# Kernel tuning notes

Hardware: AMD Instinct MI355X
Metric: run time of the kernel (lower is better)

The kernel has to match this reference:

```python
import jax, jax.numpy as jnp
import numpy as np

SIZE_IMG = 512
STRIDE = 32
N_ANCHOR = 9
BOUND_AC_LO, BOUND_AC_HI = -0.2, 1.2
EPS = 1e-05
IOU_SCALE = 10000
NEG_TH_ACGT = int(IOU_SCALE * 0.3)
POS_TH_ACGT = int(IOU_SCALE * 0.5)
POS_TH_GTAC = int(IOU_SCALE * 0.01)
NUM_POS_RPN = 128
NUM_NEG_RPN = 128
B, N_GT = 512, 32


def _anchors_rel(size_img, stride):
    h_fm = w_fm = size_img // stride
    # scales: closest floor power of 2 of min image side
    smax = 2 ** (size_img).bit_length()
    scales = np.array([smax >> 3, smax >> 2, smax >> 1], dtype=np.float32)
    sqrt2 = 1.4142135624
    ratio_hw = np.array([[sqrt2, sqrt2 / 2], [1, 1], [sqrt2 / 2, sqrt2]], dtype=np.float32)
    # (9,2) heights/widths: 3 scales x 3 ratios
    hw = (scales[:, None, None] * ratio_hw[None]).reshape(9, 2)
    ys = (np.arange(h_fm, dtype=np.float32) * stride + stride // 2)
    xs = (np.arange(w_fm, dtype=np.float32) * stride + stride // 2)
    cy = np.tile(ys[:, None, None], (1, w_fm, N_ANCHOR))
    cx = np.tile(xs[None, :, None], (h_fm, 1, N_ANCHOR))
    ctr = np.stack([cy, cx], axis=-1)                      # (H,W,9,2)
    hw_half = 0.5 * np.tile(hw[None, None], (h_fm, w_fm, 1, 1))
    ac_abs = np.concatenate([ctr - hw_half, ctr + hw_half], axis=-1).reshape(-1, 4)
    ac = ac_abs / np.float32(size_img)                     # relative (ymin,xmin,ymax,xmax)
    keep = ((ac[:, 0] >= BOUND_AC_LO) & (ac[:, 1] >= BOUND_AC_LO)
            & (ac[:, 2] <= BOUND_AC_HI) & (ac[:, 3] <= BOUND_AC_HI)
            & (ac[:, 2] > ac[:, 0]) & (ac[:, 3] > ac[:, 1]))
    return ac[keep].astype(np.float32)                     # (1384, 4)


def setup_inputs() -> dict:
    key = jax.random.key(0)
    k1, k2, k3, k4 = jax.random.split(key, 4)
    # valid GT boxes: sorted coord pairs in [0,1]
    yy = jnp.sort(jax.random.uniform(k1, (B, N_GT, 2)), axis=-1)
    xx = jnp.sort(jax.random.uniform(k2, (B, N_GT, 2)), axis=-1)
    bx_gt = jnp.stack([yy[..., 0], xx[..., 0], yy[..., 1], xx[..., 1]], axis=-1)
    ac_val = jnp.asarray(_anchors_rel(SIZE_IMG, STRIDE))
    rand_pos = jax.random.uniform(k3, (B, ac_val.shape[0]))
    rand_neg = jax.random.uniform(k4, (B, ac_val.shape[0]))
    return {"bx_gt": bx_gt, "ac_val": ac_val, "rand_pos": rand_pos, "rand_neg": rand_neg}


def _iou_mat(ac, gt):
    # ac (N_ac,4), gt (B,N_gt,4) -> (B,N_ac,N_gt)
    a = ac[None, :, None, :]
    g = gt[:, None, :, :]
    ih = jnp.clip(jnp.minimum(a[..., 2], g[..., 2]) - jnp.maximum(a[..., 0], g[..., 0]), 0.0)
    iw = jnp.clip(jnp.minimum(a[..., 3], g[..., 3]) - jnp.maximum(a[..., 1], g[..., 1]), 0.0)
    inter = ih * iw
    area_ac = (ac[:, 2] - ac[:, 0]) * (ac[:, 3] - ac[:, 1])
    area_gt = (gt[..., 2] - gt[..., 0]) * (gt[..., 3] - gt[..., 1])
    union = area_ac[None, :, None] + area_gt[:, None, :] - inter
    return inter / (union + EPS)


def _bbox2delta(bx_l, bx_r):
    h_r = jnp.maximum(bx_r[..., 2] - bx_r[..., 0], EPS)
    w_r = jnp.maximum(bx_r[..., 3] - bx_r[..., 1], EPS)
    yc_r = bx_r[..., 0] + 0.5 * (bx_r[..., 2] - bx_r[..., 0])
    xc_r = bx_r[..., 1] + 0.5 * (bx_r[..., 3] - bx_r[..., 1])
    h_l = bx_l[..., 2] - bx_l[..., 0]
    w_l = bx_l[..., 3] - bx_l[..., 1]
    yc_l = bx_l[..., 0] + 0.5 * h_l
    xc_l = bx_l[..., 1] + 0.5 * w_l
    d = jnp.stack([(xc_l - xc_r) / w_r, (yc_l - yc_r) / h_r,
                   jnp.log(w_l / w_r), jnp.log(h_l / h_r)], axis=-1)
    return jnp.clip(d, -10.0, 10.0)


def _sample_mask(mask, num, rand):
    th = num / (jnp.sum(mask, axis=-1, keepdims=True) + 1e-06)
    return jnp.where(rand < th, 1.0, 0.0) * mask


def reference(bx_gt, ac_val, rand_pos, rand_neg):
    iou = _iou_mat(ac_val, bx_gt)                          # (B, N_ac, N_gt)
    ious = (iou * IOU_SCALE).astype(jnp.int32)             # scale-integer IoU
    best_gt = jnp.argmax(ious, axis=-1)                    # (B, N_ac)
    iou_acgt = jnp.max(ious, axis=-1)                      # (B, N_ac)
    best_ac = jnp.argmax(ious, axis=1)                     # (B, N_gt)
    iou_gtac = jnp.max(ious, axis=1)                       # (B, N_gt)
    b, n_ac = iou_acgt.shape
    valid_gtac = (iou_gtac >= POS_TH_GTAC).astype(jnp.float32)
    pos_gtac = jnp.zeros((b, n_ac), jnp.float32).at[
        jnp.arange(b)[:, None], best_ac].max(valid_gtac) > 0.5
    pos = (iou_acgt >= POS_TH_ACGT) | pos_gtac             # (B, N_ac)
    neg = (iou_acgt < NEG_TH_ACGT) & (~pos)
    gt_match = bx_gt[jnp.arange(b)[:, None], best_gt]      # (B, N_ac, 4)
    bx_tgt = jnp.where(pos[..., None], gt_match,
                       jnp.where(neg[..., None], -2.0, -1.0))
    coor_sum = jnp.sum(bx_tgt, axis=-1)
    mask_fg = jnp.where(coor_sum > -4.0, 1.0, 0.0)
    mask_bg = jnp.where(coor_sum <= -8.0, 1.0, 0.0)
    mask_pos = _sample_mask(mask_fg, NUM_POS_RPN, rand_pos)
    mask_neg = _sample_mask(mask_bg, NUM_NEG_RPN, rand_neg)
    ac_b = jnp.broadcast_to(ac_val[None], bx_tgt.shape)
    bx_safe = jnp.where(pos[..., None], bx_tgt, ac_b)      # avoid log of negatives
    bx_del = _bbox2delta(bx_safe, ac_b)
    return jnp.concatenate(
        [bx_tgt, bx_del, mask_pos[..., None], mask_neg[..., None]], axis=-1)
```

## Files before the change

### kernel.cpp

```cpp
#include <hip/hip_runtime.h>

#define NGT   32
#define EPSF  1e-5f
#define GTAC_BIT (1 << 20)

__global__ __launch_bounds__(256) void rpn_k1(
    const float* __restrict__ bx_gt,
    const float* __restrict__ ac_val,
    int* __restrict__ pack,
    int* __restrict__ colkey,
    int* __restrict__ partial,
    int n_ac)
{
    #pragma clang fp contract(off)
    const int b = blockIdx.y, chunk = blockIdx.x, tid = threadIdx.x;
    const int w = tid >> 6, lane = tid & 63;

    __shared__ float s_gt[NGT * 4];
    __shared__ float s_agt[NGT];
    __shared__ int   s_wk[NGT * 4];
    __shared__ int   s_c[8];

    if (tid < NGT * 4) s_gt[tid] = bx_gt[(size_t)b * NGT * 4 + tid];
    __syncthreads();
    if (tid < NGT) {
        float g0 = s_gt[tid*4+0], g1 = s_gt[tid*4+1];
        float g2 = s_gt[tid*4+2], g3 = s_gt[tid*4+3];
        s_agt[tid] = (g2 - g0) * (g3 - g1);
    }
    __syncthreads();

    const int a = chunk * 256 + tid;
    const bool active = (a < n_ac);
    float a0 = 0.f, a1 = 0.f, a2 = 0.f, a3 = 0.f, area = 0.f;
    if (active) {
        float4 av = ((const float4*)ac_val)[a];
        a0 = av.x; a1 = av.y; a2 = av.z; a3 = av.w;
        area = (a2 - a0) * (a3 - a1);
    }

    int vmax = -1, bgt = 0;
    #pragma unroll
    for (int g = 0; g < NGT; ++g) {
        float g0 = s_gt[g*4+0], g1 = s_gt[g*4+1];
        float g2 = s_gt[g*4+2], g3 = s_gt[g*4+3];
        float ih = fmaxf(fminf(a2, g2) - fmaxf(a0, g0), 0.0f);
        float iw = fmaxf(fminf(a3, g3) - fmaxf(a1, g1), 0.0f);
        float inter = ih * iw;
        float uni = area + s_agt[g] - inter;
        float iou = inter / (uni + EPSF);
        int v = (int)(iou * 10000.0f);
        if (active && v > vmax) { vmax = v; bgt = g; }
        int key = active ? ((v << 12) | (4095 - a)) : 0;
        #pragma unroll
        for (int off = 32; off >= 1; off >>= 1)
            key = max(key, __shfl_xor(key, off, 64));
        if (lane == 0) s_wk[g*4 + w] = key;
    }

    if (active) pack[(size_t)b * n_ac + a] = (vmax << 5) | bgt;

    int cf = (active && vmax >= 5000) ? 1 : 0;
    int cb = (active && vmax < 3000 && vmax >= 0) ? 1 : 0;
    #pragma unroll
    for (int off = 32; off >= 1; off >>= 1) {
        cf += __shfl_xor(cf, off, 64);
        cb += __shfl_xor(cb, off, 64);
    }
    if (lane == 0) { s_c[w*2] = cf; s_c[w*2+1] = cb; }
    __syncthreads();

    if (tid < NGT) {
        int k = max(max(s_wk[tid*4+0], s_wk[tid*4+1]),
                    max(s_wk[tid*4+2], s_wk[tid*4+3]));
        atomicMax(&colkey[b * NGT + tid], k);
    }
    if (tid == 0) {
        partial[(b * gridDim.x + chunk) * 2 + 0] = s_c[0] + s_c[2] + s_c[4] + s_c[6];
        partial[(b * gridDim.x + chunk) * 2 + 1] = s_c[1] + s_c[3] + s_c[5] + s_c[7];
    }
}

__global__ __launch_bounds__(64) void rpn_k2(
    int* __restrict__ pack,
    const int* __restrict__ colkey,
    const int* __restrict__ partial,
    float* __restrict__ th,
    int n_ac, int n_chunk)
{
    const int b = blockIdx.x, tid = threadIdx.x;

    int pf = 0, pb = 0;
    if (tid < n_chunk) {
        pf = partial[(b * n_chunk + tid) * 2 + 0];
        pb = partial[(b * n_chunk + tid) * 2 + 1];
    }
    #pragma unroll
    for (int off = 32; off >= 1; off >>= 1) {
        pf += __shfl_xor(pf, off, 64);
        pb += __shfl_xor(pb, off, 64);
    }

    int valid = 0, a = 0;
    if (tid < NGT) {
        int key = colkey[b * NGT + tid];
        int v = key >> 12;
        a = 4095 - (key & 4095);
        valid = (v >= 100);
    }
    int av = valid ? a : (0x10000 + tid);
    bool dup = false;
    for (int gp = 0; gp < NGT; ++gp) {
        int o = __shfl(av, gp, 64);
        if (gp < tid && o == av) dup = true;
    }
    bool contrib = valid && !dup;
    int rm = 0x7FFF;
    if (contrib) rm = pack[(size_t)b * n_ac + a] >> 5;
    unsigned long long m1 = __ballot(contrib && rm < 5000);
    unsigned long long m2 = __ballot(contrib && rm < 3000);

    if (contrib) atomicOr(&pack[(size_t)b * n_ac + a], GTAC_BIT);

    if (tid == 0) {
        int cf = pf + __popcll(m1);
        int cb = pb - __popcll(m2);
        th[b*2 + 0] = 128.0f / ((float)cf + 1e-6f);
        th[b*2 + 1] = 128.0f / ((float)cb + 1e-6f);
    }
}

__global__ __launch_bounds__(256) void rpn_k3(
    const float* __restrict__ bx_gt,
    const float* __restrict__ ac_val,
    const float* __restrict__ rand_pos,
    const float* __restrict__ rand_neg,
    const int* __restrict__ pack,
    const float* __restrict__ th,
    float* __restrict__ out,
    int n_ac)
{
    #pragma clang fp contract(off)
    const int b = blockIdx.y, chunk = blockIdx.x, tid = threadIdx.x;
    __shared__ float s_gt[NGT * 4];
    if (tid < NGT * 4) s_gt[tid] = bx_gt[(size_t)b * NGT * 4 + tid];
    __syncthreads();

    const int a = chunk * 256 + tid;
    if (a >= n_ac) return;

    const float th_pos = th[b*2 + 0];
    const float th_neg = th[b*2 + 1];
    const int p = pack[(size_t)b * n_ac + a];
    const bool gtac = (p & GTAC_BIT) != 0;
    const int rm = (p >> 5) & 0x7FFF;
    const int bg = p & 31;
    const bool pos = (rm >= 5000) || gtac;
    const bool neg = !pos && (rm < 3000);

    const float4 av = ((const float4*)ac_val)[a];
    const float a0 = av.x, a1 = av.y, a2 = av.z, a3 = av.w;

    float o0, o1, o2, o3, o4, o5, o6, o7;
    if (pos) {
        float g0 = s_gt[bg*4+0], g1 = s_gt[bg*4+1];
        float g2 = s_gt[bg*4+2], g3 = s_gt[bg*4+3];
        o0 = g0; o1 = g1; o2 = g2; o3 = g3;
        float hr = fmaxf(a2 - a0, EPSF);
        float wr = fmaxf(a3 - a1, EPSF);
        float ycr = a0 + 0.5f * (a2 - a0);
        float xcr = a1 + 0.5f * (a3 - a1);
        float hl = g2 - g0, wl = g3 - g1;
        float ycl = g0 + 0.5f * hl;
        float xcl = g1 + 0.5f * wl;
        o4 = fminf(fmaxf((xcl - xcr) / wr, -10.0f), 10.0f);
        o5 = fminf(fmaxf((ycl - ycr) / hr, -10.0f), 10.0f);
        o6 = fminf(fmaxf(logf(wl / wr), -10.0f), 10.0f);
        o7 = fminf(fmaxf(logf(hl / hr), -10.0f), 10.0f);
    } else {
        float t = neg ? -2.0f : -1.0f;
        o0 = o1 = o2 = o3 = t;
        o4 = o5 = o6 = o7 = 0.0f;
    }
    const float o8 = (pos && rand_pos[(size_t)b * n_ac + a] < th_pos) ? 1.0f : 0.0f;
    const float o9 = (neg && rand_neg[(size_t)b * n_ac + a] < th_neg) ? 1.0f : 0.0f;

    float* dst = out + ((size_t)b * n_ac + a) * 10;
    dst[0] = o0; dst[1] = o1; dst[2] = o2; dst[3] = o3;
    dst[4] = o4; dst[5] = o5; dst[6] = o6; dst[7] = o7;
    dst[8] = o8; dst[9] = o9;
}

extern "C" void kernel_launch(void* const* d_in, const int* in_sizes, int n_in,
                              void* d_out, int out_size, void* d_ws, size_t ws_size,
                              hipStream_t stream) {
    const float* bx_gt    = (const float*)d_in[0];
    const float* ac_val   = (const float*)d_in[1];
    const float* rand_pos = (const float*)d_in[2];
    const float* rand_neg = (const float*)d_in[3];
    float* out = (float*)d_out;

    const int n_ac    = in_sizes[1] / 4;
    const int B       = in_sizes[2] / n_ac;
    const int n_chunk = (n_ac + 255) / 256;

    int* pack    = (int*)d_ws;
    int* colkey  = pack + (size_t)B * n_ac;
    int* partial = colkey + (size_t)B * NGT;
    float* th    = (float*)(partial + (size_t)B * n_chunk * 2);

    rpn_k1<<<dim3(n_chunk, B), 256, 0, stream>>>(bx_gt, ac_val, pack, colkey, partial, n_ac);
    rpn_k2<<<B, 64, 0, stream>>>(pack, colkey, partial, th, n_ac, n_chunk);
    rpn_k3<<<dim3(n_chunk, B), 256, 0, stream>>>(bx_gt, ac_val, rand_pos, rand_neg,
                                                 pack, th, out, n_ac);
}
```

Before: 120.3 us.

## Process three anchors per thread in IoU kernel and coalesce output stores

The IoU kernel now has each thread handle three anchors. Per-column max keys accumulate in registers, so the 32 wave-shuffle reductions run once per three anchors instead of once per anchor. GT boxes are read straight from global memory as float4, and the argmax tie-break is folded into a packed key. The output kernel stages its ten results per anchor in padded shared memory and writes them back contiguously, replacing the strided 40-byte-per-thread stores. The trade-offs are more register pressure and fewer blocks in kernel one, plus an extra barrier and shared-memory footprint in kernel three.

New measurement: 114.3 us. -5.0%, faster.

```diff
diff --git a/kernel.cpp b/kernel.cpp
--- a/kernel.cpp
+++ b/kernel.cpp
@@ -3,6 +3,8 @@
 #define NGT   32
 #define EPSF  1e-5f
 #define GTAC_BIT (1 << 20)
+#define APT   3
+#define K1SPAN (APT * 256)
 
 __global__ __launch_bounds__(256) void rpn_k1(
     const float* __restrict__ bx_gt,
@@ -16,52 +18,61 @@
     const int b = blockIdx.y, chunk = blockIdx.x, tid = threadIdx.x;
     const int w = tid >> 6, lane = tid & 63;
 
-    __shared__ float s_gt[NGT * 4];
-    __shared__ float s_agt[NGT];
-    __shared__ int   s_wk[NGT * 4];
-    __shared__ int   s_c[8];
-
-    if (tid < NGT * 4) s_gt[tid] = bx_gt[(size_t)b * NGT * 4 + tid];
-    __syncthreads();
-    if (tid < NGT) {
-        float g0 = s_gt[tid*4+0], g1 = s_gt[tid*4+1];
-        float g2 = s_gt[tid*4+2], g3 = s_gt[tid*4+3];
-        s_agt[tid] = (g2 - g0) * (g3 - g1);
-    }
-    __syncthreads();
-
-    const int a = chunk * 256 + tid;
-    const bool active = (a < n_ac);
-    float a0 = 0.f, a1 = 0.f, a2 = 0.f, a3 = 0.f, area = 0.f;
-    if (active) {
-        float4 av = ((const float4*)ac_val)[a];
-        a0 = av.x; a1 = av.y; a2 = av.z; a3 = av.w;
-        area = (a2 - a0) * (a3 - a1);
-    }
-
-    int vmax = -1, bgt = 0;
+    __shared__ int s_wk[NGT * 4];
+    __shared__ int s_c[8];
+
+    const float4* __restrict__ gtp = (const float4*)(bx_gt + (size_t)b * NGT * 4);
+
+    int ckey[NGT];
+    #pragma unroll
+    for (int g = 0; g < NGT; ++g) ckey[g] = 0;
+
+    int cf = 0, cb = 0;
+
+    for (int j = 0; j < APT; ++j) {
+        const int a = chunk * K1SPAN + j * 256 + tid;
+        const bool active = (a < n_ac);
+        float a0 = 0.f, a1 = 0.f, a2 = 0.f, a3 = 0.f;
+        if (active) {
+            float4 av = ((const float4*)ac_val)[a];
+            a0 = av.x; a1 = av.y; a2 = av.z; a3 = av.w;
+        }
+        const float area = (a2 - a0) * (a3 - a1);
+
+        int rkey = -1;
+        const int akey = active ? (4095 - a) : -1;
+        #pragma unroll
+        for (int g = 0; g < NGT; ++g) {
+            const float4 g4 = gtp[g];
+            const float area_g = (g4.z - g4.x) * (g4.w - g4.y);
+            float ih = fmaxf(fminf(a2, g4.z) - fmaxf(a0, g4.x), 0.0f);
+            float iw = fmaxf(fminf(a3, g4.w) - fmaxf(a1, g4.y), 0.0f);
+            float inter = ih * iw;
+            float uni = area + area_g - inter;
+            float iou = inter / (uni + EPSF);
+            int v = (int)(iou * 10000.0f);
+            int rk = (v << 5) | (31 - g);
+            rkey = max(rkey, rk);
+            int key = active ? ((v << 12) | (4095 - a)) : 0;
+            ckey[g] = max(ckey[g], key);
+        }
+        if (active) {
+            pack[(size_t)b * n_ac + a] = rkey;
+            const int vmax = rkey >> 5;
+            cf += (vmax >= 5000);
+            cb += (vmax < 3000);
+        }
+    }
+
     #pragma unroll
     for (int g = 0; g < NGT; ++g) {
-        float g0 = s_gt[g*4+0], g1 = s_gt[g*4+1];
-        float g2 = s_gt[g*4+2], g3 = s_gt[g*4+3];
-        float ih = fmaxf(fminf(a2, g2) - fmaxf(a0, g0), 0.0f);
-        float iw = fmaxf(fminf(a3, g3) - fmaxf(a1, g1), 0.0f);
-        float inter = ih * iw;
-        float uni = area + s_agt[g] - inter;
-        float iou = inter / (uni + EPSF);
-        int v = (int)(iou * 10000.0f);
-        if (active && v > vmax) { vmax = v; bgt = g; }
-        int key = active ? ((v << 12) | (4095 - a)) : 0;
+        int k = ckey[g];
         #pragma unroll
         for (int off = 32; off >= 1; off >>= 1)
-            key = max(key, __shfl_xor(key, off, 64));
-        if (lane == 0) s_wk[g*4 + w] = key;
-    }
-
-    if (active) pack[(size_t)b * n_ac + a] = (vmax << 5) | bgt;
-
-    int cf = (active && vmax >= 5000) ? 1 : 0;
-    int cb = (active && vmax < 3000 && vmax >= 0) ? 1 : 0;
+            k = max(k, __shfl_xor(k, off, 64));
+        if (lane == 0) s_wk[g*4 + w] = k;
+    }
+
     #pragma unroll
     for (int off = 32; off >= 1; off >>= 1) {
         cf += __shfl_xor(cf, off, 64);
@@ -142,53 +153,70 @@
 {
     #pragma clang fp contract(off)
     const int b = blockIdx.y, chunk = blockIdx.x, tid = threadIdx.x;
+
     __shared__ float s_gt[NGT * 4];
+    __shared__ float s_o[10 * 257];
+
     if (tid < NGT * 4) s_gt[tid] = bx_gt[(size_t)b * NGT * 4 + tid];
     __syncthreads();
 
     const int a = chunk * 256 + tid;
-    if (a >= n_ac) return;
-
-    const float th_pos = th[b*2 + 0];
-    const float th_neg = th[b*2 + 1];
-    const int p = pack[(size_t)b * n_ac + a];
-    const bool gtac = (p & GTAC_BIT) != 0;
-    const int rm = (p >> 5) & 0x7FFF;
-    const int bg = p & 31;
-    const bool pos = (rm >= 5000) || gtac;
-    const bool neg = !pos && (rm < 3000);
-
-    const float4 av = ((const float4*)ac_val)[a];
-    const float a0 = av.x, a1 = av.y, a2 = av.z, a3 = av.w;
-
-    float o0, o1, o2, o3, o4, o5, o6, o7;
-    if (pos) {
-        float g0 = s_gt[bg*4+0], g1 = s_gt[bg*4+1];
-        float g2 = s_gt[bg*4+2], g3 = s_gt[bg*4+3];
-        o0 = g0; o1 = g1; o2 = g2; o3 = g3;
-        float hr = fmaxf(a2 - a0, EPSF);
-        float wr = fmaxf(a3 - a1, EPSF);
-        float ycr = a0 + 0.5f * (a2 - a0);
-        float xcr = a1 + 0.5f * (a3 - a1);
-        float hl = g2 - g0, wl = g3 - g1;
-        float ycl = g0 + 0.5f * hl;
-        float xcl = g1 + 0.5f * wl;
-        o4 = fminf(fmaxf((xcl - xcr) / wr, -10.0f), 10.0f);
-        o5 = fminf(fmaxf((ycl - ycr) / hr, -10.0f), 10.0f);
-        o6 = fminf(fmaxf(logf(wl / wr), -10.0f), 10.0f);
-        o7 = fminf(fmaxf(logf(hl / hr), -10.0f), 10.0f);
-    } else {
-        float t = neg ? -2.0f : -1.0f;
-        o0 = o1 = o2 = o3 = t;
-        o4 = o5 = o6 = o7 = 0.0f;
-    }
-    const float o8 = (pos && rand_pos[(size_t)b * n_ac + a] < th_pos) ? 1.0f : 0.0f;
-    const float o9 = (neg && rand_neg[(size_t)b * n_ac + a] < th_neg) ? 1.0f : 0.0f;
-
-    float* dst = out + ((size_t)b * n_ac + a) * 10;
-    dst[0] = o0; dst[1] = o1; dst[2] = o2; dst[3] = o3;
-    dst[4] = o4; dst[5] = o5; dst[6] = o6; dst[7] = o7;
-    dst[8] = o8; dst[9] = o9;
+    if (a < n_ac) {
+        const float th_pos = th[b*2 + 0];
+        const float th_neg = th[b*2 + 1];
+        const int p = pack[(size_t)b * n_ac + a];
+        const bool gtac = (p & GTAC_BIT) != 0;
+        const int rm = (p >> 5) & 0x7FFF;
+        const int bg = 31 - (p & 31);
+        const bool pos = (rm >= 5000) || gtac;
+        const bool neg = !pos && (rm < 3000);
+
+        const float4 avv = ((const float4*)ac_val)[a];
+        const float a0 = avv.x, a1 = avv.y, a2 = avv.z, a3 = avv.w;
+
+        float o0, o1, o2, o3, o4, o5, o6, o7;
+        if (pos) {
+            float g0 = s_gt[bg*4+0], g1 = s_gt[bg*4+1];
+            float g2 = s_gt[bg*4+2], g3 = s_gt[bg*4+3];
+            o0 = g0; o1 = g1; o2 = g2; o3 = g3;
+            float hr = fmaxf(a2 - a0, EPSF);
+            float wr = fmaxf(a3 - a1, EPSF);
+            float ycr = a0 + 0.5f * (a2 - a0);
+            float xcr = a1 + 0.5f * (a3 - a1);
+            float hl = g2 - g0, wl = g3 - g1;
+            float ycl = g0 + 0.5f * hl;
+            float xcl = g1 + 0.5f * wl;
+            o4 = fminf(fmaxf((xcl - xcr) / wr, -10.0f), 10.0f);
+            o5 = fminf(fmaxf((ycl - ycr) / hr, -10.0f), 10.0f);
+            o6 = fminf(fmaxf(logf(wl / wr), -10.0f), 10.0f);
+            o7 = fminf(fmaxf(logf(hl / hr), -10.0f), 10.0f);
+        } else {
+            float t = neg ? -2.0f : -1.0f;
+            o0 = o1 = o2 = o3 = t;
+            o4 = o5 = o6 = o7 = 0.0f;
+        }
+        const float o8 = (pos && rand_pos[(size_t)b * n_ac + a] < th_pos) ? 1.0f : 0.0f;
+        const float o9 = (neg && rand_neg[(size_t)b * n_ac + a] < th_neg) ? 1.0f : 0.0f;
+
+        s_o[0*257 + tid] = o0; s_o[1*257 + tid] = o1;
+        s_o[2*257 + tid] = o2; s_o[3*257 + tid] = o3;
+        s_o[4*257 + tid] = o4; s_o[5*257 + tid] = o5;
+        s_o[6*257 + tid] = o6; s_o[7*257 + tid] = o7;
+        s_o[8*257 + tid] = o8; s_o[9*257 + tid] = o9;
+    }
+    __syncthreads();
+
+    const int na_blk = min(256, n_ac - chunk * 256);
+    const int nd = na_blk * 10;
+    float* dst = out + ((size_t)b * n_ac + (size_t)chunk * 256) * 10;
+    #pragma unroll
+    for (int m = 0; m < 10; ++m) {
+        const int idx = m * 256 + tid;
+        if (idx < nd) {
+            const int al = idx / 10, k = idx - al * 10;
+            dst[idx] = s_o[k * 257 + al];
+        }
+    }
 }
 
 extern "C" void kernel_launch(void* const* d_in, const int* in_sizes, int n_in,
@@ -200,17 +228,18 @@
     const float* rand_neg = (const float*)d_in[3];
     float* out = (float*)d_out;
 
-    const int n_ac    = in_sizes[1] / 4;
-    const int B       = in_sizes[2] / n_ac;
-    const int n_chunk = (n_ac + 255) / 256;
+    const int n_ac     = in_sizes[1] / 4;
+    const int B        = in_sizes[2] / n_ac;
+    const int n_chunk1 = (n_ac + K1SPAN - 1) / K1SPAN;
+    const int n_chunk3 = (n_ac + 255) / 256;
 
     int* pack    = (int*)d_ws;
     int* colkey  = pack + (size_t)B * n_ac;
     int* partial = colkey + (size_t)B * NGT;
-    float* th    = (float*)(partial + (size_t)B * n_chunk * 2);
-
-    rpn_k1<<<dim3(n_chunk, B), 256, 0, stream>>>(bx_gt, ac_val, pack, colkey, partial, n_ac);
-    rpn_k2<<<B, 64, 0, stream>>>(pack, colkey, partial, th, n_ac, n_chunk);
-    rpn_k3<<<dim3(n_chunk, B), 256, 0, stream>>>(bx_gt, ac_val, rand_pos, rand_neg,
-                                                 pack, th, out, n_ac);
-}
+    float* th    = (float*)(partial + (size_t)B * n_chunk1 * 2);
+
+    rpn_k1<<<dim3(n_chunk1, B), 256, 0, stream>>>(bx_gt, ac_val, pack, colkey, partial, n_ac);
+    rpn_k2<<<B, 64, 0, stream>>>(pack, colkey, partial, th, n_ac, n_chunk1);
+    rpn_k3<<<dim3(n_chunk3, B), 256, 0, stream>>>(bx_gt, ac_val, rand_pos, rand_neg,
+                                                  pack, th, out, n_ac);
+}
```
